# Kernel optimization log

Measured on AMD Instinct MI355X. Metric: run time of the kernel, lower is better.

The kernel has to match this reference:

```python
import jax, jax.numpy as jnp
import numpy as np

B, HG, WG, D, NH, K = 4, 32, 32, 768, 12, 7
HD = D // NH  # 64


def _neigh_idx(H, W, k):
    # NATTEN semantics: 7x7 window centered at the query, shifted (clamped)
    # at borders so every query has exactly k*k neighbors.
    si = np.clip(np.arange(H) - k // 2, 0, H - k)  # [H] window row starts
    sj = np.clip(np.arange(W) - k // 2, 0, W - k)  # [W] window col starts
    ri = si[:, None] + np.arange(k)[None, :]       # [H, k]
    cj = sj[:, None] + np.arange(k)[None, :]       # [W, k]
    idx = ri[:, None, :, None] * W + cj[None, :, None, :]  # [H, W, k, k]
    return jnp.asarray(idx.reshape(H * W, k * k), dtype=jnp.int32)


def setup_inputs() -> dict:
    key = jax.random.key(0)
    ks = jax.random.split(key, 3)
    s = D ** -0.5
    return {
        "x": jax.random.normal(ks[0], (B, HG * WG, D), dtype=jnp.float32),
        "qkv_w": jax.random.normal(ks[1], (3 * D, D), dtype=jnp.float32) * s,
        "qkv_b": jnp.zeros((3 * D,), dtype=jnp.float32),
        "proj_w": jax.random.normal(ks[2], (D, D), dtype=jnp.float32) * s,
        "proj_b": jnp.zeros((D,), dtype=jnp.float32),
    }


def reference(x, qkv_w, qkv_b, proj_w, proj_b):
    b, n, d = x.shape  # n == HG*WG
    idx = _neigh_idx(HG, WG, K)  # [n, K*K] flat neighbor token indices

    qkv = x @ qkv_w.T + qkv_b                      # [b, n, 3d]
    q, k, v = jnp.split(qkv, 3, axis=-1)
    q = q.reshape(b, n, NH, HD) * (HD ** -0.5)     # [b, n, h, hd]
    k = k.reshape(b, n, NH, HD)
    v = v.reshape(b, n, NH, HD)

    kn = jnp.take(k, idx, axis=1)                  # [b, n, 49, h, hd]
    vn = jnp.take(v, idx, axis=1)                  # [b, n, 49, h, hd]

    scores = jnp.einsum('bnhd,bnkhd->bnhk', q, kn)  # [b, n, h, 49]
    attn = jax.nn.softmax(scores, axis=-1)
    out = jnp.einsum('bnhk,bnkhd->bnhd', attn, vn).reshape(b, n, d)
    return out @ proj_w.T + proj_b
```

## Files before the change

kernel.cpp:

```cpp
#include <hip/hip_runtime.h>


typedef __bf16 bf16x8 __attribute__((ext_vector_type(8)));
typedef short s16x4 __attribute__((ext_vector_type(4)));
typedef float f32x4 __attribute__((ext_vector_type(4)));

__device__ __forceinline__ unsigned short f2bf(float f) {
  unsigned u = __float_as_uint(f);
  u += 0x7fffu + ((u >> 16) & 1u);
  return (unsigned short)(u >> 16);
}

template <typename T>
__device__ __forceinline__ void gld_lds16(const T* g, T* l) {
  __builtin_amdgcn_global_load_lds((const __attribute__((address_space(1))) void*)g,
                                   (__attribute__((address_space(3))) void*)l, 16, 0, 0);
}

__global__ void cvt_kernel(const float* __restrict__ x, const float* __restrict__ w1,
                           const float* __restrict__ w2, unsigned short* __restrict__ xo,
                           unsigned short* __restrict__ w1o, unsigned short* __restrict__ w2o) {
  const int n1 = 4096 * 768 / 4;
  const int n2 = 2304 * 768 / 4;
  const int n3 = 768 * 768 / 4;
  int i = blockIdx.x * 256 + threadIdx.x;
  float4 v;
  unsigned short* dst;
  int o;
  if (i < n1) {
    o = i; v = ((const float4*)x)[o]; dst = xo;
  } else if (i < n1 + n2) {
    o = i - n1; v = ((const float4*)w1)[o]; dst = w1o;
  } else if (i < n1 + n2 + n3) {
    o = i - n1 - n2; v = ((const float4*)w2)[o]; dst = w2o;
  } else {
    return;
  }
  ushort4 r;
  r.x = f2bf(v.x); r.y = f2bf(v.y); r.z = f2bf(v.z); r.w = f2bf(v.w);
  ((ushort4*)dst)[o] = r;
}

template <int MODE, int BM, int BN>
__global__ __launch_bounds__(256, 4) void gemm_bt(const unsigned short* __restrict__ A,
                                                  const unsigned short* __restrict__ Bm,
                                                  const float* __restrict__ bias,
                                                  unsigned short* __restrict__ obf,
                                                  unsigned short* __restrict__ vtout,
                                                  float* __restrict__ of32,
                                                  int M, int N, int Kd) {
  constexpr int RA = BM / 64, RB = BN / 64;
  constexpr int MI = BM / 32, NI = BN / 32;
  constexpr int NB = (MODE == 0) ? 4 : 5;
  constexpr int DEPTH = NB - 1;
  __shared__ __align__(16) unsigned short sA[NB][BM * 32];
  __shared__ __align__(16) unsigned short sB[NB][BN * 32];
  const int tid = threadIdx.x;
  const int lane = tid & 63;
  const int wv = tid >> 6;

  constexpr int HX = (MODE == 0) ? 18 : 6;
  constexpr int HY = 16;
  const int lin = blockIdx.y * gridDim.x + blockIdx.x;
  const int xcd = lin & 7, rrr = lin >> 3;
  const int bx = (xcd & 1) * HX + rrr % HX;
  const int by = (xcd >> 1) * HY + rrr / HX;
  const int m0 = by * BM, n0 = bx * BN;

  const int wrow = (wv >> 1) * (BM / 2), wcol = (wv & 1) * (BN / 2);
  const int lr = lane & 15, lq = lane >> 4;
  const int rchunk = (lq ^ ((lr >> 1) & 3)) * 8;

  f32x4 acc[MI][NI] = {};

  const int schunk = ((tid & 3) ^ ((tid >> 3) & 3)) * 8;
  const unsigned short* gA = A + (size_t)(m0 + (tid >> 2)) * Kd + schunk;
  const unsigned short* gB = Bm + (size_t)(n0 + (tid >> 2)) * Kd + schunk;

  const int NS = Kd >> 5;

#define STAGE_TILE(tile, bufidx)                                                          \
  do {                                                                                    \
    const int _off = (tile) * 32;                                                         \
    unsigned short* _dA = sA[(bufidx)];                                                   \
    unsigned short* _dB = sB[(bufidx)];                                                   \
    _Pragma("unroll")                                                                     \
    for (int _r = 0; _r < RA; ++_r)                                                       \
      gld_lds16(gA + (size_t)(_r * 64) * Kd + _off, _dA + _r * 2048 + tid * 8);           \
    _Pragma("unroll")                                                                     \
    for (int _r = 0; _r < RB; ++_r)                                                       \
      gld_lds16(gB + (size_t)(_r * 64) * Kd + _off, _dB + _r * 2048 + tid * 8);           \
  } while (0)

#pragma unroll
  for (int t = 0; t < DEPTH; ++t) STAGE_TILE(t, t);
  __builtin_amdgcn_sched_barrier(0);
  if constexpr (MODE == 0) asm volatile("s_waitcnt vmcnt(4) lgkmcnt(0)" ::: "memory");
  else                     asm volatile("s_waitcnt vmcnt(6) lgkmcnt(0)" ::: "memory");
  __builtin_amdgcn_s_barrier();

  int rb = 0, sb = DEPTH;
  for (int step = 0; step < NS; ++step) {
    const unsigned short* cA = sA[rb];
    const unsigned short* cB = sB[rb];
    bf16x8 af[MI], bfr[NI];
#pragma unroll
    for (int t = 0; t < MI; ++t) af[t] = *(const bf16x8*)(cA + (wrow + t * 16 + lr) * 32 + rchunk);
#pragma unroll
    for (int t = 0; t < NI; ++t) bfr[t] = *(const bf16x8*)(cB + (wcol + t * 16 + lr) * 32 + rchunk);

    if (step + DEPTH < NS) STAGE_TILE(step + DEPTH, sb);

#pragma unroll
    for (int im = 0; im < MI; ++im)
#pragma unroll
      for (int in = 0; in < NI; ++in)
        acc[im][in] = __builtin_amdgcn_mfma_f32_16x16x32_bf16(af[im], bfr[in], acc[im][in], 0, 0, 0);

    __builtin_amdgcn_sched_barrier(0);
    if constexpr (MODE == 0) {
      if (step + 3 < NS)      asm volatile("s_waitcnt vmcnt(4) lgkmcnt(0)" ::: "memory");
      else if (step + 2 < NS) asm volatile("s_waitcnt vmcnt(2) lgkmcnt(0)" ::: "memory");
      else                    asm volatile("s_waitcnt vmcnt(0) lgkmcnt(0)" ::: "memory");
    } else {
      if (step + 4 < NS)      asm volatile("s_waitcnt vmcnt(6) lgkmcnt(0)" ::: "memory");
      else if (step + 3 < NS) asm volatile("s_waitcnt vmcnt(4) lgkmcnt(0)" ::: "memory");
      else if (step + 2 < NS) asm volatile("s_waitcnt vmcnt(2) lgkmcnt(0)" ::: "memory");
      else                    asm volatile("s_waitcnt vmcnt(0) lgkmcnt(0)" ::: "memory");
    }
    __builtin_amdgcn_s_barrier();
    rb = (rb + 1 == NB) ? 0 : rb + 1;
    sb = (sb + 1 == NB) ? 0 : sb + 1;
  }
#undef STAGE_TILE

  if (MODE == 0) {
    const int sidx = n0 / 768;
    if (sidx == 2) {
#pragma unroll
      for (int im = 0; im < MI; ++im) {
#pragma unroll
        for (int in = 0; in < NI; ++in) {
          int gn = n0 + wcol + in * 16 + lr;
          int rem = gn - 1536;
          int hh = rem >> 6, dd = gn & 63;
          float bsv = bias[gn];
          int gm0 = m0 + wrow + im * 16 + lq * 4;
          ushort4 pk;
          pk.x = f2bf(acc[im][in][0] + bsv);
          pk.y = f2bf(acc[im][in][1] + bsv);
          pk.z = f2bf(acc[im][in][2] + bsv);
          pk.w = f2bf(acc[im][in][3] + bsv);
          *(ushort4*)(vtout + (size_t)(hh * 64 + dd) * 4096 + gm0) = pk;
        }
      }
    } else {
      const float scale = (sidx == 0) ? 0.18033688f : 1.0f;
#pragma unroll
      for (int im = 0; im < MI; ++im) {
#pragma unroll
        for (int in = 0; in < NI; ++in) {
          int gn = n0 + wcol + in * 16 + lr;
          int rem = gn - sidx * 768;
          int hh = rem >> 6, dd = gn & 63;
          float bsv = bias[gn];
#pragma unroll
          for (int r = 0; r < 4; ++r) {
            int gm = m0 + wrow + im * 16 + lq * 4 + r;
            float val = (acc[im][in][r] + bsv) * scale;
            obf[((size_t)(sidx * 12 + hh) * 4096 + gm) * 64 + dd] = f2bf(val);
          }
        }
      }
    }
  } else {
#pragma unroll
    for (int im = 0; im < MI; ++im) {
#pragma unroll
      for (int in = 0; in < NI; ++in) {
        int gn = n0 + wcol + in * 16 + lr;
        float bsv = bias[gn];
#pragma unroll
        for (int r = 0; r < 4; ++r) {
          int gm = m0 + wrow + im * 16 + lq * 4 + r;
          of32[(size_t)gm * N + gn] = acc[im][in][r] + bsv;
        }
      }
    }
  }
}

__global__ __launch_bounds__(256, 2) void natten_kernel(const unsigned short* __restrict__ qkvt,
                                                        unsigned short* __restrict__ aout) {
  __shared__ __align__(16) unsigned short sQ[64 * 64];
  __shared__ __align__(16) unsigned short sK[256 * 64];
  __shared__ __align__(16) unsigned short sVt[64 * 256];
  const int h = blockIdx.x, ip = blockIdx.y, b = blockIdx.z;
  const int i0 = ip * 2;
  const int tid = threadIdx.x, lane = tid & 63, wv = tid >> 6;
  const int lg = lane >> 4, lm = lane & 15;
  int si0 = i0 - 3; si0 = si0 < 0 ? 0 : si0; if (si0 > 25) si0 = 25;
  const int gb = b * 1024;
  const unsigned short* Qg = qkvt + ((size_t)h * 4096 + gb + i0 * 32) * 64;
  const unsigned short* Kg = qkvt + ((size_t)(12 + h) * 4096 + gb) * 64;
  const unsigned short* Vg = qkvt + (size_t)24 * 4096 * 64 + (size_t)h * 64 * 4096 + gb;

#pragma unroll
  for (int it = 0; it < 2; ++it) {
    int f = it * 256 + tid;
    int q = f >> 3, c16 = f & 7;
    uint4 v = *(const uint4*)(Qg + q * 64 + c16 * 8);
    int s = q & 15;
    *(uint2*)(sQ + q * 64 + ((((c16 << 1)) ^ s) << 2)) = make_uint2(v.x, v.y);
    *(uint2*)(sQ + q * 64 + ((((c16 << 1) | 1) ^ s) << 2)) = make_uint2(v.z, v.w);
  }
#pragma unroll
  for (int it = 0; it < 8; ++it) {
    int f = it * 256 + tid;
    int t = f >> 3, c16 = f & 7;
    int wr = t >> 5, c = t & 31;
    int row = si0 + wr; if (row > 31) row = 31;
    uint4 v = *(const uint4*)(Kg + (row * 32 + c) * 64 + c16 * 8);
    int s = t & 15;
    *(uint2*)(sK + t * 64 + ((((c16 << 1)) ^ s) << 2)) = make_uint2(v.x, v.y);
    *(uint2*)(sK + t * 64 + ((((c16 << 1) | 1) ^ s) << 2)) = make_uint2(v.z, v.w);
  }
#pragma unroll
  for (int it = 0; it < 8; ++it) {
    int f = it * 256 + tid;
    int d = f >> 5, tc16 = f & 31;
    int wr = tc16 >> 2;
    int row = si0 + wr; if (row > 31) row = 31;
    uint4 v = *(const uint4*)(Vg + (size_t)d * 4096 + row * 32 + (tc16 & 3) * 8);
    int s = d & 15;
    *(uint2*)(sVt + d * 256 + ((((tc16 << 1)) ^ s) << 2)) = make_uint2(v.x, v.y);
    *(uint2*)(sVt + d * 256 + ((((tc16 << 1) | 1) ^ s) << 2)) = make_uint2(v.z, v.w);
  }
  __syncthreads();

  const int row_sel = wv >> 1;
  const int jhalf = wv & 1;
  const int i = i0 + row_sel;
  int si_w = i - 3; si_w = si_w < 0 ? 0 : si_w; if (si_w > 25) si_w = 25;
  const int toff = (si_w - si0) * 32;
  const int j = jhalf * 16 + lm;
  int sj = j - 3; sj = sj < 0 ? 0 : sj; if (sj > 25) sj = 25;

  float madd[2][4];
#pragma unroll
  for (int p = 0; p < 2; ++p)
#pragma unroll
    for (int r = 0; r < 4; ++r) {
      int c = p * 16 + lg * 4 + r;
      madd[p][r] = (c >= sj && c <= sj + 6) ? 0.f : -1e30f;
    }

  s16x4 qf[4];
  const int qrow = row_sel * 32 + j;
#pragma unroll
  for (int ks = 0; ks < 4; ++ks)
    qf[ks] = *(const s16x4*)(sQ + qrow * 64 + ((((ks << 2) + lg) ^ (qrow & 15)) << 2));

  f32x4 accS[14];
#pragma unroll
  for (int tt = 0; tt < 14; ++tt) {
    f32x4 a = {0.f, 0.f, 0.f, 0.f};
    const int trow = toff + tt * 16 + lm;
    const unsigned short* kr = sK + trow * 64;
    const int sw = trow & 15;
#pragma unroll
    for (int ks = 0; ks < 4; ++ks) {
      s16x4 kf = *(const s16x4*)(kr + ((((ks << 2) + lg) ^ sw) << 2));
      a = __builtin_amdgcn_mfma_f32_16x16x16bf16_1k(kf, qf[ks], a, 0, 0, 0);
    }
    accS[tt] = a;
  }

  float mx = -3e38f;
#pragma unroll
  for (int tt = 0; tt < 14; ++tt)
#pragma unroll
    for (int r = 0; r < 4; ++r) {
      float v = accS[tt][r] + madd[tt & 1][r];
      accS[tt][r] = v;
      mx = fmaxf(mx, v);
    }
  mx = fmaxf(mx, __shfl_xor(mx, 16, 64));
  mx = fmaxf(mx, __shfl_xor(mx, 32, 64));
  float sum = 0.f;
#pragma unroll
  for (int tt = 0; tt < 14; ++tt)
#pragma unroll
    for (int r = 0; r < 4; ++r) {
      float p = exp2f(accS[tt][r] - mx);
      accS[tt][r] = p;
      sum += p;
    }
  sum += __shfl_xor(sum, 16, 64);
  sum += __shfl_xor(sum, 32, 64);
  const float inv = 1.f / sum;

  s16x4 pf[14];
#pragma unroll
  for (int tt = 0; tt < 14; ++tt) {
    union { unsigned u[2]; s16x4 v; } pk;
    pk.u[0] = ((unsigned)f2bf(accS[tt][1]) << 16) | f2bf(accS[tt][0]);
    pk.u[1] = ((unsigned)f2bf(accS[tt][3]) << 16) | f2bf(accS[tt][2]);
    pf[tt] = pk.v;
  }

  f32x4 accO[4] = {};
  const int choff = toff >> 2;
#pragma unroll
  for (int tt = 0; tt < 14; ++tt) {
    const int c8 = choff + tt * 4 + lg;
#pragma unroll
    for (int nt = 0; nt < 4; ++nt) {
      const int d = nt * 16 + lm;
      s16x4 vf = *(const s16x4*)(sVt + d * 256 + ((c8 ^ (d & 15)) << 2));
      accO[nt] = __builtin_amdgcn_mfma_f32_16x16x16bf16_1k(pf[tt], vf, accO[nt], 0, 0, 0);
    }
  }

  float invr[4];
#pragma unroll
  for (int r = 0; r < 4; ++r) invr[r] = __shfl(inv, lg * 4 + r, 64);

  const int tokbase = gb + i * 32 + jhalf * 16;
#pragma unroll
  for (int nt = 0; nt < 4; ++nt)
#pragma unroll
    for (int r = 0; r < 4; ++r) {
      int tok = tokbase + lg * 4 + r;
      aout[(size_t)tok * 768 + h * 64 + nt * 16 + lm] = f2bf(accO[nt][r] * invr[r]);
    }
}

extern "C" void kernel_launch(void* const* d_in, const int* in_sizes, int n_in,
                              void* d_out, int out_size, void* d_ws, size_t ws_size,
                              hipStream_t stream) {
  const float* x      = (const float*)d_in[0];
  const float* qkv_w  = (const float*)d_in[1];
  const float* qkv_b  = (const float*)d_in[2];
  const float* proj_w = (const float*)d_in[3];
  const float* proj_b = (const float*)d_in[4];
  char* ws = (char*)d_ws;

  unsigned short* xb    = (unsigned short*)(ws);
  unsigned short* wqkv  = (unsigned short*)(ws + 6291456);
  unsigned short* wproj = (unsigned short*)(ws + 9830400);
  unsigned short* qkvt  = (unsigned short*)(ws + 11010048);
  unsigned short* attnb = (unsigned short*)(ws + 29884416);
  unsigned short* vt    = qkvt + (size_t)24 * 4096 * 64;
  float* out = (float*)d_out;

  cvt_kernel<<<5376, 256, 0, stream>>>(x, qkv_w, proj_w, xb, wqkv, wproj);
  gemm_bt<0, 64, 64><<<dim3(36, 64), 256, 0, stream>>>(xb, wqkv, qkv_b, qkvt, vt, nullptr, 4096, 2304, 768);
  natten_kernel<<<dim3(12, 16, 4), 256, 0, stream>>>(qkvt, attnb);
  gemm_bt<1, 64, 64><<<dim3(12, 64), 256, 0, stream>>>(attnb, wproj, proj_b, nullptr, nullptr, out, 4096, 768, 768);
}
```

Baseline: 144.7 us.

## Replace QKV GEMM with 256x256-tile 512-thread kernel using swizzled LDS

```diff
diff --git a/kernel.cpp b/kernel.cpp
--- a/kernel.cpp
+++ b/kernel.cpp
@@ -41,14 +41,137 @@
   ((ushort4*)dst)[o] = r;
 }
 
+__global__ __launch_bounds__(512, 1) void gemm_qkv3(const unsigned short* __restrict__ A,
+                                                    const unsigned short* __restrict__ Bm,
+                                                    const float* __restrict__ bias,
+                                                    unsigned short* __restrict__ obf,
+                                                    unsigned short* __restrict__ vtout) {
+  __shared__ __align__(16) unsigned short sA[3][256 * 32];
+  __shared__ __align__(16) unsigned short sB[3][256 * 32];
+  const int tid = threadIdx.x, lane = tid & 63, wv = tid >> 6;
+  const int wr = wv >> 2, wc = wv & 3;
+  const int lr = lane & 15, lq = lane >> 4;
+
+  const int lin = blockIdx.x;
+  const int wgid = (lin & 7) * 18 + (lin >> 3);
+  const int bx = wgid % 9, by = wgid / 9;
+  const int m0 = by * 256, n0 = bx * 256;
+
+  const int srow = tid >> 2;
+  const int pchunk = (tid & 3) * 8;
+  const int swz = (srow & 3) ^ ((srow >> 2) & 3);
+  const unsigned short* gA = A + (size_t)(m0 + srow) * 768 + ((tid & 3) ^ swz) * 8;
+  const unsigned short* gB = Bm + (size_t)(n0 + srow) * 768 + ((tid & 3) ^ swz) * 8;
+  const int ldst = srow * 32 + pchunk;
+
+  const int fsw = (lq ^ (lr & 3) ^ ((lr >> 2) & 3)) * 8;
+
+  f32x4 acc[8][4] = {};
+
+#define STG(t2, ld)                                                                           \
+  do {                                                                                        \
+    unsigned short* d = (((ld) < 2) ? sA[(t2) % 3] : sB[(t2) % 3]) +                          \
+                        ((((ld) & 1) != 0) ? 128 * 32 : 0) + ldst;                            \
+    const unsigned short* g = (((ld) < 2) ? gA : gB) +                                        \
+                              ((((ld) & 1) != 0) ? (size_t)128 * 768 : (size_t)0) + (t2) * 32;\
+    gld_lds16(g, d);                                                                          \
+  } while (0)
+
+#define QPHASE(mfb, ld)                                                                       \
+  do {                                                                                        \
+    bf16x8 a0 = *(const bf16x8*)(cA + (wr * 128 + (mfb) * 16 + lr) * 32 + fsw);               \
+    bf16x8 a1 = *(const bf16x8*)(cA + (wr * 128 + ((mfb) + 1) * 16 + lr) * 32 + fsw);         \
+    if (stg) STG(t + 2, ld);                                                                  \
+    __builtin_amdgcn_s_barrier();                                                             \
+    __builtin_amdgcn_s_setprio(1);                                                            \
+    _Pragma("unroll")                                                                         \
+    for (int nf = 0; nf < 4; ++nf) {                                                          \
+      acc[(mfb)][nf] =                                                                        \
+          __builtin_amdgcn_mfma_f32_16x16x32_bf16(a0, bfr[nf], acc[(mfb)][nf], 0, 0, 0);      \
+      acc[(mfb) + 1][nf] =                                                                    \
+          __builtin_amdgcn_mfma_f32_16x16x32_bf16(a1, bfr[nf], acc[(mfb) + 1][nf], 0, 0, 0);  \
+    }                                                                                         \
+    __builtin_amdgcn_s_setprio(0);                                                            \
+  } while (0)
+
+  STG(0, 0); STG(0, 1); STG(0, 2); STG(0, 3);
+  STG(1, 0); STG(1, 1); STG(1, 2); STG(1, 3);
+  __builtin_amdgcn_sched_barrier(0);
+  asm volatile("s_waitcnt vmcnt(4)" ::: "memory");
+  __builtin_amdgcn_s_barrier();
+
+  for (int t = 0; t < 24; ++t) {
+    const unsigned short* cA = sA[t % 3];
+    const unsigned short* cB = sB[t % 3];
+    const bool stg = (t + 2 < 24);
+    bf16x8 bfr[4];
+#pragma unroll
+    for (int nf = 0; nf < 4; ++nf)
+      bfr[nf] = *(const bf16x8*)(cB + (wc * 64 + nf * 16 + lr) * 32 + fsw);
+
+    QPHASE(0, 0);
+    __builtin_amdgcn_s_barrier();
+    QPHASE(2, 1);
+    __builtin_amdgcn_s_barrier();
+    QPHASE(4, 2);
+    __builtin_amdgcn_s_barrier();
+    QPHASE(6, 3);
+    __builtin_amdgcn_sched_barrier(0);
+    if (t < 22)       asm volatile("s_waitcnt vmcnt(4)" ::: "memory");
+    else if (t == 22) asm volatile("s_waitcnt vmcnt(0)" ::: "memory");
+    __builtin_amdgcn_s_barrier();
+  }
+#undef QPHASE
+#undef STG
+
+  const int sidx = n0 / 768;
+  if (sidx == 2) {
+#pragma unroll
+    for (int mf = 0; mf < 8; ++mf) {
+#pragma unroll
+      for (int nf = 0; nf < 4; ++nf) {
+        int gn = n0 + wc * 64 + nf * 16 + lr;
+        int rem = gn - 1536;
+        int hh = rem >> 6, dd = gn & 63;
+        float bsv = bias[gn];
+        int gm0 = m0 + wr * 128 + mf * 16 + lq * 4;
+        ushort4 pk;
+        pk.x = f2bf(acc[mf][nf][0] + bsv);
+        pk.y = f2bf(acc[mf][nf][1] + bsv);
+        pk.z = f2bf(acc[mf][nf][2] + bsv);
+        pk.w = f2bf(acc[mf][nf][3] + bsv);
+        *(ushort4*)(vtout + (size_t)(hh * 64 + dd) * 4096 + gm0) = pk;
+      }
+    }
+  } else {
+    const float scale = (sidx == 0) ? 0.18033688f : 1.0f;
+#pragma unroll
+    for (int mf = 0; mf < 8; ++mf) {
+#pragma unroll
+      for (int nf = 0; nf < 4; ++nf) {
+        int gn = n0 + wc * 64 + nf * 16 + lr;
+        int rem = gn - sidx * 768;
+        int hh = rem >> 6, dd = gn & 63;
+        float bsv = bias[gn];
+#pragma unroll
+        for (int r = 0; r < 4; ++r) {
+          int gm = m0 + wr * 128 + mf * 16 + lq * 4 + r;
+          float val = (acc[mf][nf][r] + bsv) * scale;
+          obf[((size_t)(sidx * 12 + hh) * 4096 + gm) * 64 + dd] = f2bf(val);
+        }
+      }
+    }
+  }
+}
+
 template <int MODE, int BM, int BN>
-__global__ __launch_bounds__(256, 4) void gemm_bt(const unsigned short* __restrict__ A,
-                                                  const unsigned short* __restrict__ Bm,
-                                                  const float* __restrict__ bias,
-                                                  unsigned short* __restrict__ obf,
-                                                  unsigned short* __restrict__ vtout,
-                                                  float* __restrict__ of32,
-                                                  int M, int N, int Kd) {
+__global__ __launch_bounds__(256) void gemm_bt(const unsigned short* __restrict__ A,
+                                               const unsigned short* __restrict__ Bm,
+                                               const float* __restrict__ bias,
+                                               unsigned short* __restrict__ obf,
+                                               unsigned short* __restrict__ vtout,
+                                               float* __restrict__ of32,
+                                               int M, int N, int Kd) {
   constexpr int RA = BM / 64, RB = BN / 64;
   constexpr int MI = BM / 32, NI = BN / 32;
   constexpr int NB = (MODE == 0) ? 4 : 5;
@@ -95,8 +218,7 @@
 #pragma unroll
   for (int t = 0; t < DEPTH; ++t) STAGE_TILE(t, t);
   __builtin_amdgcn_sched_barrier(0);
-  if constexpr (MODE == 0) asm volatile("s_waitcnt vmcnt(4) lgkmcnt(0)" ::: "memory");
-  else                     asm volatile("s_waitcnt vmcnt(6) lgkmcnt(0)" ::: "memory");
+  asm volatile("s_waitcnt vmcnt(6) lgkmcnt(0)" ::: "memory");
   __builtin_amdgcn_s_barrier();
 
   int rb = 0, sb = DEPTH;
@@ -118,73 +240,26 @@
         acc[im][in] = __builtin_amdgcn_mfma_f32_16x16x32_bf16(af[im], bfr[in], acc[im][in], 0, 0, 0);
 
     __builtin_amdgcn_sched_barrier(0);
-    if constexpr (MODE == 0) {
-      if (step + 3 < NS)      asm volatile("s_waitcnt vmcnt(4) lgkmcnt(0)" ::: "memory");
-      else if (step + 2 < NS) asm volatile("s_waitcnt vmcnt(2) lgkmcnt(0)" ::: "memory");
-      else                    asm volatile("s_waitcnt vmcnt(0) lgkmcnt(0)" ::: "memory");
-    } else {
-      if (step + 4 < NS)      asm volatile("s_waitcnt vmcnt(6) lgkmcnt(0)" ::: "memory");
-      else if (step + 3 < NS) asm volatile("s_waitcnt vmcnt(4) lgkmcnt(0)" ::: "memory");
-      else if (step + 2 < NS) asm volatile("s_waitcnt vmcnt(2) lgkmcnt(0)" ::: "memory");
-      else                    asm volatile("s_waitcnt vmcnt(0) lgkmcnt(0)" ::: "memory");
-    }
+    if (step + 4 < NS)      asm volatile("s_waitcnt vmcnt(6) lgkmcnt(0)" ::: "memory");
+    else if (step + 3 < NS) asm volatile("s_waitcnt vmcnt(4) lgkmcnt(0)" ::: "memory");
+    else if (step + 2 < NS) asm volatile("s_waitcnt vmcnt(2) lgkmcnt(0)" ::: "memory");
+    else                    asm volatile("s_waitcnt vmcnt(0) lgkmcnt(0)" ::: "memory");
     __builtin_amdgcn_s_barrier();
     rb = (rb + 1 == NB) ? 0 : rb + 1;
     sb = (sb + 1 == NB) ? 0 : sb + 1;
   }
 #undef STAGE_TILE
 
-  if (MODE == 0) {
-    const int sidx = n0 / 768;
-    if (sidx == 2) {
-#pragma unroll
-      for (int im = 0; im < MI; ++im) {
-#pragma unroll
-        for (int in = 0; in < NI; ++in) {
-          int gn = n0 + wcol + in * 16 + lr;
-          int rem = gn - 1536;
-          int hh = rem >> 6, dd = gn & 63;
-          float bsv = bias[gn];
-          int gm0 = m0 + wrow + im * 16 + lq * 4;
-          ushort4 pk;
-          pk.x = f2bf(acc[im][in][0] + bsv);
-          pk.y = f2bf(acc[im][in][1] + bsv);
-          pk.z = f2bf(acc[im][in][2] + bsv);
-          pk.w = f2bf(acc[im][in][3] + bsv);
-          *(ushort4*)(vtout + (size_t)(hh * 64 + dd) * 4096 + gm0) = pk;
-        }
-      }
-    } else {
-      const float scale = (sidx == 0) ? 0.18033688f : 1.0f;
-#pragma unroll
-      for (int im = 0; im < MI; ++im) {
-#pragma unroll
-        for (int in = 0; in < NI; ++in) {
-          int gn = n0 + wcol + in * 16 + lr;
-          int rem = gn - sidx * 768;
-          int hh = rem >> 6, dd = gn & 63;
-          float bsv = bias[gn];
-#pragma unroll
-          for (int r = 0; r < 4; ++r) {
-            int gm = m0 + wrow + im * 16 + lq * 4 + r;
-            float val = (acc[im][in][r] + bsv) * scale;
-            obf[((size_t)(sidx * 12 + hh) * 4096 + gm) * 64 + dd] = f2bf(val);
-          }
-        }
-      }
-    }
-  } else {
-#pragma unroll
-    for (int im = 0; im < MI; ++im) {
-#pragma unroll
-      for (int in = 0; in < NI; ++in) {
-        int gn = n0 + wcol + in * 16 + lr;
-        float bsv = bias[gn];
-#pragma unroll
-        for (int r = 0; r < 4; ++r) {
-          int gm = m0 + wrow + im * 16 + lq * 4 + r;
-          of32[(size_t)gm * N + gn] = acc[im][in][r] + bsv;
-        }
+#pragma unroll
+  for (int im = 0; im < MI; ++im) {
+#pragma unroll
+    for (int in = 0; in < NI; ++in) {
+      int gn = n0 + wcol + in * 16 + lr;
+      float bsv = bias[gn];
+#pragma unroll
+      for (int r = 0; r < 4; ++r) {
+        int gm = m0 + wrow + im * 16 + lq * 4 + r;
+        of32[(size_t)gm * N + gn] = acc[im][in][r] + bsv;
       }
     }
   }
@@ -355,7 +430,7 @@
   float* out = (float*)d_out;
 
   cvt_kernel<<<5376, 256, 0, stream>>>(x, qkv_w, proj_w, xb, wqkv, wproj);
-  gemm_bt<0, 64, 64><<<dim3(36, 64), 256, 0, stream>>>(xb, wqkv, qkv_b, qkvt, vt, nullptr, 4096, 2304, 768);
+  gemm_qkv3<<<144, 512, 0, stream>>>(xb, wqkv, qkv_b, qkvt, vt);
   natten_kernel<<<dim3(12, 16, 4), 256, 0, stream>>>(qkvt, attnb);
   gemm_bt<1, 64, 64><<<dim3(12, 64), 256, 0, stream>>>(attnb, wproj, proj_b, nullptr, nullptr, out, 4096, 768, 768);
 }
```

Result: no change. 143.5 us (-0.8%).
